# Optimization experiments

Measured on AMD Instinct MI355X. Metric: run time of the kernel, lower is better.

The kernel has to match this reference:

```python
import jax, jax.numpy as jnp
import numpy as np

LN_EPS = 1e-5

def conv2d(x, w, b, padding, dilation=1):
    # x: [B,C,H,W], w: [O,I,kh,kw] (torch OIHW layout)
    y = jax.lax.conv_general_dilated(
        x, w, window_strides=(1, 1),
        padding=[(padding, padding), (padding, padding)],
        rhs_dilation=(dilation, dilation),
        dimension_numbers=('NCHW', 'OIHW', 'NCHW'))
    return y + b[None, :, None, None]

def layer_norm(x, w, b):
    # normalize over (C,H,W) like nn.LayerNorm([C,15,15])
    mu = jnp.mean(x, axis=(1, 2, 3), keepdims=True)
    var = jnp.var(x, axis=(1, 2, 3), keepdims=True)
    return (x - mu) * jax.lax.rsqrt(var + LN_EPS) * w[None] + b[None]

def setup_inputs() -> dict:
    key = jax.random.key(0)
    B, C, H, W, S = 256, 256, 15, 15, 8
    ks = jax.random.split(key, 20)
    def w_conv(k, kh, kw):
        fan_in = C * kh * kw
        bound = 1.0 / np.sqrt(fan_in)
        return jax.random.uniform(k, (C, C, kh, kw), jnp.float32, -bound, bound)
    def w_fusion(k):
        fan_in = 4 * C
        bound = 1.0 / np.sqrt(fan_in)
        return jax.random.uniform(k, (C, 4 * C, 1, 1), jnp.float32, -bound, bound)
    def bias(k, fan_in, n=None):
        bound = 1.0 / np.sqrt(fan_in)
        return jax.random.uniform(k, (n if n is not None else C,), jnp.float32, -bound, bound)
    return {
        'x': jax.random.normal(ks[0], (B, C, H, W), jnp.float32),
        'spiking_probabilities': jax.random.uniform(ks[1], (S,), jnp.float32),
        'w3': w_conv(ks[2], 3, 3), 'b3': bias(ks[3], C * 9),
        'w3d': w_conv(ks[4], 3, 3), 'b3d': bias(ks[5], C * 9),
        'w5': w_conv(ks[6], 5, 5), 'b5': bias(ks[7], C * 25),
        'w7': w_conv(ks[8], 7, 7), 'b7': bias(ks[9], C * 49),
        'wf': w_fusion(ks[10]), 'bf': bias(ks[11], 4 * C),
        'w1': w_conv(ks[12], 1, 1), 'b1': bias(ks[13], C),
        'ln_w': jnp.ones((C, H, W), jnp.float32),
        'ln_b': jnp.zeros((C, H, W), jnp.float32),
        'step_param': jax.random.uniform(ks[14], (S,), jnp.float32),
        'spike_scale': jax.random.uniform(ks[15], (S,), jnp.float32),
        'residual_weights': jax.random.uniform(ks[16], (S,), jnp.float32),
    }

def reference(x, spiking_probabilities, w3, b3, w3d, b3d, w5, b5, w7, b7,
              wf, bf, w1, b1, ln_w, ln_b, step_param, spike_scale, residual_weights):
    elu = jax.nn.elu
    # multi-scale perception
    dx3 = elu(conv2d(x, w3, b3, padding=1))
    dx3d = elu(conv2d(x, w3d, b3d, padding=2, dilation=2))
    dx5 = elu(conv2d(x, w5, b5, padding=2))
    dx7 = elu(conv2d(x, w7, b7, padding=3))
    xf = elu(conv2d(jnp.concatenate([dx3, dx3d, dx5, dx7], axis=1), wf, bf, padding=0))

    base_key = jax.random.key(42)
    num_steps = step_param.shape[0]

    def step(xc, inp):
        sp, ss, rw, prob, i = inp
        dx = elu(layer_norm(conv2d(xc, w1, b1, padding=0), ln_w, ln_b))
        v = jnp.var(dx, axis=(1, 2, 3), ddof=1)  # torch.var unbiased
        noise = jax.random.uniform(jax.random.fold_in(base_key, i), xc.shape, xc.dtype)
        x_new = xc + dx * sp + noise * prob * ss + xc * rw
        return x_new, v

    xs = (step_param, spike_scale, residual_weights,
          spiking_probabilities, jnp.arange(num_steps))
    x_final, vs = jax.lax.scan(step, xf, xs)
    nca_var = vs.T  # [B, num_steps]
    return (x_final, nca_var)
```

## Files before the change

kernel.cpp:

```cpp
#include <hip/hip_runtime.h>
#include <cstdint>

constexpr int B_ = 256, C_ = 256, H_ = 15, W_ = 15, P_ = 225, S_ = 8;
constexpr int CHW = C_ * P_;
constexpr size_t NX = (size_t)B_ * CHW;

typedef __attribute__((ext_vector_type(8))) short short8v;
typedef __attribute__((ext_vector_type(4))) float float4v;
typedef __attribute__((ext_vector_type(16))) float float16v;

__host__ __device__ inline void tf2x32(uint32_t k0, uint32_t k1,
                                       uint32_t x0, uint32_t x1,
                                       uint32_t& o0, uint32_t& o1) {
  uint32_t ks[3] = {k0, k1, k0 ^ k1 ^ 0x1BD11BDAu};
  const uint32_t rot0[4] = {13u, 15u, 26u, 6u};
  const uint32_t rot1[4] = {17u, 29u, 16u, 24u};
  x0 += ks[0]; x1 += ks[1];
#pragma unroll
  for (int r = 0; r < 5; ++r) {
    const uint32_t* rr = (r & 1) ? rot1 : rot0;
#pragma unroll
    for (int j = 0; j < 4; ++j) {
      x0 += x1;
      x1 = (x1 << rr[j]) | (x1 >> (32 - rr[j]));
      x1 ^= x0;
    }
    x0 += ks[(r + 1) % 3];
    x1 += ks[(r + 2) % 3] + (uint32_t)(r + 1);
  }
  o0 = x0; o1 = x1;
}

__device__ inline float tf_uniform(uint32_t bits) {
  return __uint_as_float((bits >> 9) | 0x3F800000u) - 1.0f;
}

__device__ inline float elu1(float v) { return v > 0.f ? v : expm1f(v); }

__device__ inline unsigned short f2bf(float f) {
  uint32_t u = __float_as_uint(f);
  return (unsigned short)((u + 0x7FFFu + ((u >> 16) & 1u)) >> 16);
}
__device__ inline float bf2f(unsigned short h) {
  return __uint_as_float(((uint32_t)h) << 16);
}

template <int KS, int DIL, int OFF>
__global__ void __launch_bounds__(256, 2) conv_mfma(
    const unsigned short* __restrict__ xbf, const unsigned short* __restrict__ wt,
    const float* __restrict__ bias, unsigned short* __restrict__ dxg) {
  constexpr int KS2 = KS * KS, WP = W_ + 2 * OFF, PP = WP * (H_ + 2 * OFF);
  __shared__ __align__(16) unsigned short lsA[4 * PP * 8];
  __shared__ __align__(16) unsigned short lsB[2][4 * 128 * 8];
  const int b = blockIdx.x, nh = blockIdx.y;
  const int t = threadIdx.x, wv = t >> 6, l = t & 63;
  const int m32 = l & 31, kh8 = l >> 5;
  for (int i = t; i < 4 * PP * 8; i += 256) lsA[i] = 0;
  int rbase[2];
#pragma unroll
  for (int mt = 0; mt < 2; ++mt) {
    int m = (wv * 2 + mt) * 32 + m32;
    int pc = m < P_ ? m : P_ - 1;
    int ph = pc / 15, pw = pc - 15 * ph;
    rbase[mt] = ph * WP + pw;
  }
  float16v acc[2][4];
#pragma unroll
  for (int mt = 0; mt < 2; ++mt)
#pragma unroll
    for (int nt = 0; nt < 4; ++nt)
#pragma unroll
      for (int r = 0; r < 16; ++r) acc[mt][nt][r] = 0.f;
  const unsigned short* xb = xbf + (size_t)b * P_ * 256;
  const int bl = ((t & 3) * 128 + (t >> 2)) * 8;
  const unsigned short* wbase = wt + nh * 4096;
  for (int cb = 0; cb < 8; ++cb) {
    const unsigned short* wcb = wbase + (size_t)(cb * KS2) * 8192;
    for (int i = t; i < 900; i += 256) {
      int p = i >> 2, pl = i & 3;
      short8v v = *(const short8v*)(xb + p * 256 + cb * 32 + pl * 8);
      int ph = p / 15, pw = p - 15 * ph;
      *(short8v*)&lsA[(pl * PP + (ph + OFF) * WP + pw + OFF) * 8] = v;
    }
    {
      short8v v0 = *(const short8v*)(wcb + t * 8);
      short8v v1 = *(const short8v*)(wcb + 2048 + t * 8);
      *(short8v*)&lsB[0][bl] = v0;
      *(short8v*)&lsB[0][bl + 512] = v1;
    }
    __syncthreads();
    for (int d = 0; d < KS2; ++d) {
      short8v nb0, nb1;
      const bool pre = (d + 1 < KS2);
      if (pre) {
        nb0 = *(const short8v*)(wcb + (size_t)(d + 1) * 8192 + t * 8);
        nb1 = *(const short8v*)(wcb + (size_t)(d + 1) * 8192 + 2048 + t * 8);
      }
      const unsigned short* bb = lsB[d & 1];
      const int kh = d / KS, kw = d - KS * kh;
      const int doff = DIL * (kh * WP + kw);
#pragma unroll
      for (int k16 = 0; k16 < 2; ++k16) {
        const int pl = k16 * 2 + kh8;
        short8v af[2], bfr[4];
#pragma unroll
        for (int mt = 0; mt < 2; ++mt)
          af[mt] = *(const short8v*)&lsA[(pl * PP + rbase[mt] + doff) * 8];
#pragma unroll
        for (int nt = 0; nt < 4; ++nt)
          bfr[nt] = *(const short8v*)&bb[(pl * 128 + nt * 32 + m32) * 8];
#pragma unroll
        for (int mt = 0; mt < 2; ++mt)
#pragma unroll
          for (int nt = 0; nt < 4; ++nt)
            acc[mt][nt] = __builtin_amdgcn_mfma_f32_32x32x16_bf16(
                af[mt], bfr[nt], acc[mt][nt], 0, 0, 0);
      }
      if (pre) {
        unsigned short* bw = lsB[(d + 1) & 1];
        *(short8v*)&bw[bl] = nb0;
        *(short8v*)&bw[bl + 512] = nb1;
      }
      __syncthreads();
    }
  }
#pragma unroll
  for (int nt = 0; nt < 4; ++nt) {
    int o = nh * 128 + nt * 32 + m32;
    float bv = bias[o];
#pragma unroll
    for (int mt = 0; mt < 2; ++mt) {
#pragma unroll
      for (int r = 0; r < 16; ++r) {
        int pixel = (wv * 2 + mt) * 32 + 8 * (r >> 2) + (r & 3) + 4 * kh8;
        if (pixel < P_)
          dxg[((size_t)(b * P_ + pixel)) * 256 + o] = f2bf(elu1(acc[mt][nt][r] + bv));
      }
    }
  }
}

__global__ void __launch_bounds__(512, 4) gemm_kc(
    const unsigned short* __restrict__ A0, const unsigned short* __restrict__ A1,
    const float* __restrict__ Af, int nkb,
    const unsigned short* __restrict__ Bw, const float* __restrict__ bias,
    float* __restrict__ xc, unsigned short* __restrict__ ybf,
    float* __restrict__ stats, int mode) {
  __shared__ __align__(16) unsigned short lsA[4 * P_ * 8];
  __shared__ __align__(16) unsigned short lsB[4 * 128 * 8];
  __shared__ float red[16];
  const int b = blockIdx.x, nh = blockIdx.y;
  const int t = threadIdx.x, wv = t >> 6, l = t & 63;
  const int m32 = l & 31, kh8 = l >> 5;
  const int mp = wv & 3, nq = wv >> 2;
  int prow[2];
#pragma unroll
  for (int mt = 0; mt < 2; ++mt) {
    int m = (mp * 2 + mt) * 32 + m32;
    prow[mt] = m < P_ ? m : P_ - 1;
  }
  float16v acc[2][2];
#pragma unroll
  for (int mt = 0; mt < 2; ++mt)
#pragma unroll
    for (int nt = 0; nt < 2; ++nt)
#pragma unroll
      for (int r = 0; r < 16; ++r) acc[mt][nt][r] = 0.f;
  const float* Afb = Af ? Af + (size_t)b * P_ * 256 : nullptr;
  for (int kb = 0; kb < nkb; ++kb) {
    __syncthreads();
    if (Af) {
      for (int i = t; i < 900; i += 512) {
        int p = i >> 2, pl = i & 3;
        const float* src = Afb + (size_t)p * 256 + kb * 32 + pl * 8;
        float4v f0 = *(const float4v*)src;
        float4v f1 = *(const float4v*)(src + 4);
        short8v v;
        v[0] = (short)f2bf(f0[0]); v[1] = (short)f2bf(f0[1]);
        v[2] = (short)f2bf(f0[2]); v[3] = (short)f2bf(f0[3]);
        v[4] = (short)f2bf(f1[0]); v[5] = (short)f2bf(f1[1]);
        v[6] = (short)f2bf(f1[2]); v[7] = (short)f2bf(f1[3]);
        *(short8v*)&lsA[(pl * P_ + p) * 8] = v;
      }
    } else {
      const unsigned short* Asb =
          ((kb & 8) ? A1 : A0) + (size_t)b * P_ * 256;
      for (int i = t; i < 900; i += 512) {
        int p = i >> 2, pl = i & 3;
        short8v v = *(const short8v*)(Asb + (size_t)p * 256 + (kb & 7) * 32 + pl * 8);
        *(short8v*)&lsA[(pl * P_ + p) * 8] = v;
      }
    }
    {
      short8v v = *(const short8v*)(Bw + (size_t)kb * 8192 + nh * 4096 + t * 8);
      *(short8v*)&lsB[((t & 3) * 128 + (t >> 2)) * 8] = v;
    }
    __syncthreads();
#pragma unroll
    for (int k16 = 0; k16 < 2; ++k16) {
      const int pl = k16 * 2 + kh8;
      short8v af[2], bfr[2];
#pragma unroll
      for (int mt = 0; mt < 2; ++mt)
        af[mt] = *(const short8v*)&lsA[(pl * P_ + prow[mt]) * 8];
#pragma unroll
      for (int nt = 0; nt < 2; ++nt)
        bfr[nt] = *(const short8v*)&lsB[(pl * 128 + (nq * 2 + nt) * 32 + m32) * 8];
#pragma unroll
      for (int mt = 0; mt < 2; ++mt)
#pragma unroll
        for (int nt = 0; nt < 2; ++nt)
          acc[mt][nt] = __builtin_amdgcn_mfma_f32_32x32x16_bf16(
              af[mt], bfr[nt], acc[mt][nt], 0, 0, 0);
    }
  }
  float s1 = 0.f, s2 = 0.f;
#pragma unroll
  for (int nt = 0; nt < 2; ++nt) {
    int o = nh * 128 + (nq * 2 + nt) * 32 + m32;
    float bv = bias ? bias[o] : 0.f;
#pragma unroll
    for (int mt = 0; mt < 2; ++mt) {
#pragma unroll
      for (int r = 0; r < 16; ++r) {
        int pixel = (mp * 2 + mt) * 32 + 8 * (r >> 2) + (r & 3) + 4 * kh8;
        if (pixel >= P_) continue;
        size_t idx = ((size_t)(b * P_ + pixel)) * 256 + o;
        float v = acc[mt][nt][r];
        if (mode == 0) {
          xc[idx] = v;
        } else if (mode == 2) {
          xc[idx] = elu1(xc[idx] + v + bv);
        } else {
          v += bv;
          ybf[idx] = f2bf(v);
          s1 += v;
          s2 = fmaf(v, v, s2);
        }
      }
    }
  }
  if (mode == 3) {
#pragma unroll
    for (int off = 32; off; off >>= 1) {
      s1 += __shfl_down(s1, off, 64);
      s2 += __shfl_down(s2, off, 64);
    }
    if (l == 0) { red[wv] = s1; red[8 + wv] = s2; }
    __syncthreads();
    if (t == 0) {
      float a = 0.f, c2 = 0.f;
#pragma unroll
      for (int w = 0; w < 8; ++w) { a += red[w]; c2 += red[8 + w]; }
      stats[nh * 512 + b] = a;
      stats[nh * 512 + 256 + b] = c2;
    }
  }
}

__global__ void __launch_bounds__(512) step_fused(
    const unsigned short* __restrict__ ybf, float* __restrict__ xc,
    unsigned short* __restrict__ xcbf, const float* __restrict__ stats,
    const float* __restrict__ lnwT, const float* __restrict__ lnbT,
    const float* __restrict__ sp_a, const float* __restrict__ ss_a,
    const float* __restrict__ rw_a, const float* __restrict__ prob_a,
    int s, uint32_t k0, uint32_t k1, int last, float* __restrict__ vout) {
  __shared__ float red[16];
  const int b = blockIdx.x, t = threadIdx.x;
  const float mean = (stats[b] + stats[512 + b]) * (1.0f / 57600.0f);
  const float var =
      (stats[256 + b] + stats[768 + b]) * (1.0f / 57600.0f) - mean * mean;
  const float rstd = rsqrtf(var + 1e-5f);
  const float sp = sp_a[s], pss = prob_a[s] * ss_a[s], rw1 = 1.0f + rw_a[s];
  float s1 = 0.f, s2 = 0.f;
  const size_t base = (size_t)b * CHW;
  for (int g = t; g < 7200; g += 512) {
    int i0 = g * 8;
    int p = i0 >> 8, c0 = i0 & 255;
    size_t idx = base + i0;
    short8v yv = *(const short8v*)(ybf + idx);
    float4v x0 = *(const float4v*)(xc + idx);
    float4v x1 = *(const float4v*)(xc + idx + 4);
    float4v lw0 = *(const float4v*)(lnwT + i0);
    float4v lw1 = *(const float4v*)(lnwT + i0 + 4);
    float4v lb0 = *(const float4v*)(lnbT + i0);
    float4v lb1 = *(const float4v*)(lnbT + i0 + 4);
    const uint32_t jbase = (uint32_t)b * 57600u + (uint32_t)c0 * 225u + (uint32_t)p;
    float4v o0, o1;
    short8v ob;
#pragma unroll
    for (int e = 0; e < 8; ++e) {
      float y = bf2f((unsigned short)yv[e]);
      float lw = e < 4 ? lw0[e] : lw1[e - 4];
      float lb = e < 4 ? lb0[e] : lb1[e - 4];
      float xo = e < 4 ? x0[e] : x1[e - 4];
      float dx = elu1(fmaf((y - mean) * rstd, lw, lb));
      s1 += dx;
      s2 = fmaf(dx, dx, s2);
      uint32_t y0, y1;
      tf2x32(k0, k1, 0u, jbase + 225u * (uint32_t)e, y0, y1);
      float n = tf_uniform(y0 ^ y1);
      float xn = fmaf(xo, rw1, fmaf(dx, sp, n * pss));
      if (e < 4) o0[e] = xn; else o1[e - 4] = xn;
      ob[e] = (short)f2bf(xn);
    }
    *(float4v*)(xc + idx) = o0;
    *(float4v*)(xc + idx + 4) = o1;
    if (!last) *(short8v*)(xcbf + idx) = ob;
  }
  int wv = t >> 6, l = t & 63;
#pragma unroll
  for (int off = 32; off; off >>= 1) {
    s1 += __shfl_down(s1, off, 64);
    s2 += __shfl_down(s2, off, 64);
  }
  if (l == 0) { red[wv] = s1; red[8 + wv] = s2; }
  __syncthreads();
  if (t == 0) {
    float a = 0.f, c2 = 0.f;
#pragma unroll
    for (int w = 0; w < 8; ++w) { a += red[w]; c2 += red[8 + w]; }
    float mv = a * (1.0f / 57600.0f);
    vout[b * 8 + s] = (c2 - 57600.0f * mv * mv) * (1.0f / 57599.0f);
  }
}

__global__ void __launch_bounds__(256) prep_x(const float* __restrict__ x,
                                              unsigned short* __restrict__ xbf) {
  __shared__ unsigned short ts[64 * 232];
  const int b = blockIdx.x, c0 = blockIdx.y * 64;
  const float* xs = x + ((size_t)b * 256 + c0) * P_;
  for (int i = threadIdx.x; i < 64 * P_; i += 256) {
    int c = i / P_, p = i - P_ * c;
    ts[c * 232 + p] = f2bf(xs[c * P_ + p]);
  }
  __syncthreads();
  for (int i = threadIdx.x; i < 64 * P_; i += 256) {
    int p = i >> 6, c = i & 63;
    xbf[((size_t)b * P_ + p) * 256 + c0 + c] = ts[c * 232 + p];
  }
}

__global__ void wt_prep(const float* __restrict__ w, unsigned short* __restrict__ wt,
                        int ks2) {
  int i = blockIdx.x * 256 + threadIdx.x;
  if (i >= 65536 * ks2) return;
  int cl = i & 31, o = (i >> 5) & 255, cbd = i >> 13;
  int d = cbd % ks2, cb = cbd / ks2;
  wt[i] = f2bf(w[((size_t)(o * 256) + cb * 32 + cl) * ks2 + d]);
}

__global__ void wk_prep(const float* __restrict__ w, unsigned short* __restrict__ wt,
                        int K) {
  int i = blockIdx.x * 256 + threadIdx.x;
  if (i >= K * 256) return;
  int kc = i & 31, o = (i >> 5) & 255, kb = i >> 13;
  wt[i] = f2bf(w[(size_t)o * K + kb * 32 + kc]);
}

__global__ void ln_tr(const float* __restrict__ lw, const float* __restrict__ lb,
                      float* __restrict__ ow, float* __restrict__ ob) {
  int p = blockIdx.x, c = threadIdx.x;
  ow[p * 256 + c] = lw[c * P_ + p];
  ob[p * 256 + c] = lb[c * P_ + p];
}

__global__ void __launch_bounds__(256) final_tr(const float* __restrict__ xc,
                                                float* __restrict__ out) {
  __shared__ float ts[64][226];
  const int b = blockIdx.x, c0 = blockIdx.y * 64;
  for (int i = threadIdx.x; i < 64 * P_; i += 256) {
    int cl = i & 63, p = i >> 6;
    ts[cl][p] = xc[((size_t)(b * P_ + p)) * 256 + c0 + cl];
  }
  __syncthreads();
  for (int i = threadIdx.x; i < 64 * P_; i += 256) {
    int cl = i / P_, p = i - P_ * cl;
    out[((size_t)(b * 256 + c0 + cl)) * P_ + p] = ts[cl][p];
  }
}

extern "C" void kernel_launch(void* const* d_in, const int* in_sizes, int n_in,
                              void* d_out, int out_size, void* d_ws,
                              size_t ws_size, hipStream_t stream) {
  const float* x = (const float*)d_in[0];
  const float* prob = (const float*)d_in[1];
  const float* w3 = (const float*)d_in[2];
  const float* b3 = (const float*)d_in[3];
  const float* w3d = (const float*)d_in[4];
  const float* b3d = (const float*)d_in[5];
  const float* w5 = (const float*)d_in[6];
  const float* b5 = (const float*)d_in[7];
  const float* w7 = (const float*)d_in[8];
  const float* b7 = (const float*)d_in[9];
  const float* wf = (const float*)d_in[10];
  const float* bfus = (const float*)d_in[11];
  const float* w1 = (const float*)d_in[12];
  const float* b1 = (const float*)d_in[13];
  const float* lnw = (const float*)d_in[14];
  const float* lnb = (const float*)d_in[15];
  const float* sp = (const float*)d_in[16];
  const float* ss = (const float*)d_in[17];
  const float* rw = (const float*)d_in[18];
  float* out = (float*)d_out;

  unsigned short* dxg0 = (unsigned short*)d_ws;
  unsigned short* dxg1 = (unsigned short*)((char*)d_ws + 29491200);
  float* xc = (float*)((char*)d_ws + 58982400);
  unsigned short* xcbf = dxg0;
  unsigned short* ybf = dxg1;

  char* sc = (char*)d_out;
  unsigned short* wT3 = (unsigned short*)(sc + 0);
  unsigned short* wT3d = (unsigned short*)(sc + 1179648);
  unsigned short* wT5 = (unsigned short*)(sc + 2359296);
  unsigned short* wT7 = (unsigned short*)(sc + 5636096);
  unsigned short* wfT = (unsigned short*)(sc + 12058624);
  unsigned short* w1T = (unsigned short*)(sc + 12582912);
  float* lnwT = (float*)(sc + 12713984);
  float* lnbT = (float*)(sc + 12944384);
  unsigned short* xbf = (unsigned short*)(sc + 13174784);
  float* stats = (float*)(sc + 42665984);

  prep_x<<<dim3(B_, 4), 256, 0, stream>>>(x, xbf);
  wt_prep<<<(65536 * 9 + 255) / 256, 256, 0, stream>>>(w3, wT3, 9);
  wt_prep<<<(65536 * 9 + 255) / 256, 256, 0, stream>>>(w3d, wT3d, 9);
  wt_prep<<<(65536 * 25 + 255) / 256, 256, 0, stream>>>(w5, wT5, 25);
  wt_prep<<<(65536 * 49 + 255) / 256, 256, 0, stream>>>(w7, wT7, 49);
  wk_prep<<<1024, 256, 0, stream>>>(wf, wfT, 1024);
  wk_prep<<<256, 256, 0, stream>>>(w1, w1T, 256);
  ln_tr<<<P_, 256, 0, stream>>>(lnw, lnb, lnwT, lnbT);

  conv_mfma<3, 1, 1><<<dim3(B_, 2), 256, 0, stream>>>(xbf, wT3, b3, dxg0);
  conv_mfma<3, 2, 2><<<dim3(B_, 2), 256, 0, stream>>>(xbf, wT3d, b3d, dxg1);
  gemm_kc<<<dim3(B_, 2), 512, 0, stream>>>(dxg0, dxg1, nullptr, 16, wfT,
                                           nullptr, xc, nullptr, nullptr, 0);
  conv_mfma<5, 1, 2><<<dim3(B_, 2), 256, 0, stream>>>(xbf, wT5, b5, dxg0);
  conv_mfma<7, 1, 3><<<dim3(B_, 2), 256, 0, stream>>>(xbf, wT7, b7, dxg1);
  gemm_kc<<<dim3(B_, 2), 512, 0, stream>>>(dxg0, dxg1, nullptr, 16, wfT + 131072,
                                           bfus, xc, nullptr, nullptr, 2);

  gemm_kc<<<dim3(B_, 2), 512, 0, stream>>>(nullptr, nullptr, xc, 8, w1T, b1,
                                           nullptr, ybf, stats, 3);
  for (int si = 0; si < S_; ++si) {
    uint32_t k0s, k1s;
    tf2x32(0u, 42u, 0u, (uint32_t)si, k0s, k1s);
    step_fused<<<B_, 512, 0, stream>>>(ybf, xc, xcbf, stats, lnwT, lnbT, sp, ss, rw,
                                       prob, si, k0s, k1s, si == S_ - 1, out + NX);
    if (si < S_ - 1)
      gemm_kc<<<dim3(B_, 2), 512, 0, stream>>>(xcbf, xcbf, nullptr, 8, w1T, b1,
                                               nullptr, ybf, stats, 3);
  }

  final_tr<<<dim3(B_, 4), 256, 0, stream>>>(xc, out);
}
```

Baseline: 1.703 ms.

## Batch three conv taps per LDS weight stage to cut barrier count

```diff
diff --git a/kernel.cpp b/kernel.cpp
--- a/kernel.cpp
+++ b/kernel.cpp
@@ -50,8 +50,9 @@
     const unsigned short* __restrict__ xbf, const unsigned short* __restrict__ wt,
     const float* __restrict__ bias, unsigned short* __restrict__ dxg) {
   constexpr int KS2 = KS * KS, WP = W_ + 2 * OFF, PP = WP * (H_ + 2 * OFF);
+  constexpr int NCH = (KS2 + 2) / 3;
   __shared__ __align__(16) unsigned short lsA[4 * PP * 8];
-  __shared__ __align__(16) unsigned short lsB[2][4 * 128 * 8];
+  __shared__ __align__(16) unsigned short lsB[2][3 * 4 * 128 * 8];
   const int b = blockIdx.x, nh = blockIdx.y;
   const int t = threadIdx.x, wv = t >> 6, l = t & 63;
   const int m32 = l & 31, kh8 = l >> 5;
@@ -72,33 +73,46 @@
 #pragma unroll
       for (int r = 0; r < 16; ++r) acc[mt][nt][r] = 0.f;
   const unsigned short* xb = xbf + (size_t)b * P_ * 256;
-  const int bl = ((t & 3) * 128 + (t >> 2)) * 8;
   const unsigned short* wbase = wt + nh * 4096;
-  for (int cb = 0; cb < 8; ++cb) {
-    const unsigned short* wcb = wbase + (size_t)(cb * KS2) * 8192;
-    for (int i = t; i < 900; i += 256) {
-      int p = i >> 2, pl = i & 3;
-      short8v v = *(const short8v*)(xb + p * 256 + cb * 32 + pl * 8);
-      int ph = p / 15, pw = p - 15 * ph;
-      *(short8v*)&lsA[(pl * PP + (ph + OFF) * WP + pw + OFF) * 8] = v;
-    }
-    {
-      short8v v0 = *(const short8v*)(wcb + t * 8);
-      short8v v1 = *(const short8v*)(wcb + 2048 + t * 8);
-      *(short8v*)&lsB[0][bl] = v0;
-      *(short8v*)&lsB[0][bl + 512] = v1;
-    }
-    __syncthreads();
-    for (int d = 0; d < KS2; ++d) {
-      short8v nb0, nb1;
-      const bool pre = (d + 1 < KS2);
-      if (pre) {
-        nb0 = *(const short8v*)(wcb + (size_t)(d + 1) * 8192 + t * 8);
-        nb1 = *(const short8v*)(wcb + (size_t)(d + 1) * 8192 + 2048 + t * 8);
-      }
-      const unsigned short* bb = lsB[d & 1];
+  for (int i = t; i < 900; i += 256) {
+    int p = i >> 2, pl = i & 3;
+    short8v v = *(const short8v*)(xb + p * 256 + pl * 8);
+    int ph = p / 15, pw = p - 15 * ph;
+    *(short8v*)&lsA[(pl * PP + (ph + OFF) * WP + pw + OFF) * 8] = v;
+  }
+#pragma unroll
+  for (int j = 0; j < 3; ++j) {
+    short8v v0 = *(const short8v*)(wbase + (size_t)j * 8192 + t * 8);
+    short8v v1 = *(const short8v*)(wbase + (size_t)j * 8192 + 2048 + t * 8);
+    *(short8v*)&lsB[0][((j * 4 + (t & 3)) * 128 + (t >> 2)) * 8] = v0;
+    *(short8v*)&lsB[0][((j * 4 + (t & 3)) * 128 + 64 + (t >> 2)) * 8] = v1;
+  }
+  __syncthreads();
+  for (int chk = 0; chk < 8 * NCH; ++chk) {
+    const int cb = chk / NCH;
+    const int c0 = (chk - cb * NCH) * 3;
+    const int dn = (KS2 - c0) < 3 ? (KS2 - c0) : 3;
+    const int cur = chk & 1;
+    const bool hasNext = (chk + 1) < 8 * NCH;
+    const int ncb = (chk + 1) / NCH;
+    const int nc0 = ((chk + 1) - ncb * NCH) * 3;
+    const int ndn = hasNext ? ((KS2 - nc0) < 3 ? (KS2 - nc0) : 3) : 0;
+    const bool cross = hasNext && (ncb != cb);
+    short8v nb0[3], nb1[3];
+    if (hasNext) {
+      const unsigned short* wn = wbase + ((size_t)ncb * KS2 + nc0) * 8192;
+#pragma unroll
+      for (int j = 0; j < 3; ++j)
+        if (j < ndn) {
+          nb0[j] = *(const short8v*)(wn + (size_t)j * 8192 + t * 8);
+          nb1[j] = *(const short8v*)(wn + (size_t)j * 8192 + 2048 + t * 8);
+        }
+    }
+    auto mfma_d = [&](int dd) {
+      const int d = c0 + dd;
       const int kh = d / KS, kw = d - KS * kh;
       const int doff = DIL * (kh * WP + kw);
+      const unsigned short* bb = lsB[cur] + dd * 4096;
 #pragma unroll
       for (int k16 = 0; k16 < 2; ++k16) {
         const int pl = k16 * 2 + kh8;
@@ -116,10 +130,27 @@
             acc[mt][nt] = __builtin_amdgcn_mfma_f32_32x32x16_bf16(
                 af[mt], bfr[nt], acc[mt][nt], 0, 0, 0);
       }
-      if (pre) {
-        unsigned short* bw = lsB[(d + 1) & 1];
-        *(short8v*)&bw[bl] = nb0;
-        *(short8v*)&bw[bl + 512] = nb1;
+    };
+    __builtin_amdgcn_s_setprio(1);
+    mfma_d(0);
+    if (dn == 3) { mfma_d(1); mfma_d(2); }
+    __builtin_amdgcn_s_setprio(0);
+    if (hasNext) {
+      unsigned short* bw = lsB[cur ^ 1];
+#pragma unroll
+      for (int j = 0; j < 3; ++j)
+        if (j < ndn) {
+          *(short8v*)&bw[((j * 4 + (t & 3)) * 128 + (t >> 2)) * 8] = nb0[j];
+          *(short8v*)&bw[((j * 4 + (t & 3)) * 128 + 64 + (t >> 2)) * 8] = nb1[j];
+        }
+    }
+    __syncthreads();
+    if (cross) {
+      for (int i = t; i < 900; i += 256) {
+        int p = i >> 2, pl = i & 3;
+        short8v v = *(const short8v*)(xb + p * 256 + ncb * 32 + pl * 8);
+        int ph = p / 15, pw = p - 15 * ph;
+        *(short8v*)&lsA[(pl * PP + (ph + OFF) * WP + pw + OFF) * 8] = v;
       }
       __syncthreads();
     }
```

Measured after the change: 1.688 ms. Within noise of the previous version (-0.9%).
